# Kernel optimization log

Measured on AMD Instinct MI355X. Metric: run time of the kernel, lower is better.

## Reference

```python
import jax, jax.numpy as jnp
import numpy as np


def setup_inputs() -> dict:
    key = jax.random.key(0)
    k1, k2 = jax.random.split(key)
    B, Lp, Lw, D = 4, 256, 200, 768
    bert_emb = jax.random.normal(k1, (B, Lp, D), dtype=jnp.float32)
    # pieces2word[b, w, p] == 1 iff wordpiece p belongs to word w
    pieces2word = jax.random.randint(k2, (B, Lw, Lp), 0, 2, dtype=jnp.int32)
    return {"bert_emb": bert_emb, "pieces2word": pieces2word}


def reference(bert_emb, pieces2word):
    # Faithful to EmbeddingLayer.forward:
    #   min_value = bert_emb.min().item()  (a detached scalar in torch)
    #   _bert_embs = bert_emb.unsqueeze(1).expand(-1, Lw, -1, -1)
    #   masked_fill where pieces2word == 0 with min_value; max over piece dim
    min_value = jax.lax.stop_gradient(jnp.min(bert_emb))
    # [B, Lw, Lp, D] broadcast, masked, reduced over pieces (axis=2)
    masked = jnp.where(pieces2word[:, :, :, None] != 0,
                       bert_emb[:, None, :, :],
                       min_value)
    word_reps = jnp.max(masked, axis=2)  # [B, Lw, D]
    return word_reps
```

## Files before the change

kernel.cpp:

```cpp
#include <hip/hip_runtime.h>
#include <hip/hip_bf16.h>


#define B_  4
#define LP_ 256
#define LW_ 200
#define D_  768
#define D4_ (D_ / 4)

__device__ __forceinline__ unsigned int enc_f32(float f) {
    unsigned int b = __float_as_uint(f);
    return (b & 0x80000000u) ? ~b : (b | 0x80000000u);
}
__device__ __forceinline__ float dec_f32(unsigned int u) {
    unsigned int b = (u & 0x80000000u) ? (u & 0x7FFFFFFFu) : ~u;
    return __uint_as_float(b);
}

__global__ void init_ws(unsigned int* ws) {
    if (threadIdx.x == 0) ws[0] = 0xFFFFFFFFu;
}

__global__ void min_reduce(const float4* __restrict__ x, int n4, unsigned int* ws) {
    float m = __uint_as_float(0x7F800000u);
    for (int i = blockIdx.x * blockDim.x + threadIdx.x; i < n4;
         i += gridDim.x * blockDim.x) {
        float4 v = x[i];
        m = fminf(m, fminf(fminf(v.x, v.y), fminf(v.z, v.w)));
    }
    #pragma unroll
    for (int off = 32; off > 0; off >>= 1)
        m = fminf(m, __shfl_down(m, off, 64));
    __shared__ float sm[4];
    int lane = threadIdx.x & 63, wid = threadIdx.x >> 6;
    if (lane == 0) sm[wid] = m;
    __syncthreads();
    if (threadIdx.x == 0) {
        float bm = sm[0];
        int nw = blockDim.x >> 6;
        for (int w = 1; w < nw; ++w) bm = fminf(bm, sm[w]);
        atomicMin(ws, enc_f32(bm));
    }
}

__device__ __forceinline__ float4 max4(float4 a, float4 b) {
    return make_float4(fmaxf(a.x, b.x), fmaxf(a.y, b.y),
                       fmaxf(a.z, b.z), fmaxf(a.w, b.w));
}

__global__ __launch_bounds__(192) void word_max(
    const float* __restrict__ emb, const int* __restrict__ p2w,
    const unsigned int* __restrict__ ws, float* __restrict__ out)
{
    const int bw = blockIdx.x;
    const int b = bw / LW_;
    const int w = bw - b * LW_;

    __shared__ int   active[LP_];
    __shared__ int   s_cnt;
    __shared__ float s_minv;
    if (threadIdx.x == 0) { s_cnt = 0; s_minv = dec_f32(ws[0]); }
    __syncthreads();

    const int* mrow = p2w + (b * LW_ + w) * LP_;
    for (int p = threadIdx.x; p < LP_; p += blockDim.x) {
        if (mrow[p] != 0) {
            int slot = atomicAdd(&s_cnt, 1);
            active[slot] = p;
        }
    }
    __syncthreads();

    const float  minv = s_minv;
    const int    n    = s_cnt;
    const int    dv   = threadIdx.x;
    const float4* erow = (const float4*)(emb + b * LP_ * D_);

    float4 acc = make_float4(minv, minv, minv, minv);

    int i = 0;
    for (; i + 4 <= n; i += 4) {
        int p0 = active[i + 0];
        int p1 = active[i + 1];
        int p2 = active[i + 2];
        int p3 = active[i + 3];
        float4 v0 = erow[p0 * D4_ + dv];
        float4 v1 = erow[p1 * D4_ + dv];
        float4 v2 = erow[p2 * D4_ + dv];
        float4 v3 = erow[p3 * D4_ + dv];
        acc = max4(acc, max4(max4(v0, v1), max4(v2, v3)));
    }
    for (; i < n; ++i) {
        acc = max4(acc, erow[active[i] * D4_ + dv]);
    }

    ((float4*)out)[(b * LW_ + w) * D4_ + dv] = acc;
}

extern "C" void kernel_launch(void* const* d_in, const int* in_sizes, int n_in,
                              void* d_out, int out_size, void* d_ws, size_t ws_size,
                              hipStream_t stream) {
    const float* emb = (const float*)d_in[0];
    const int*   p2w = (const int*)d_in[1];
    float*       out = (float*)d_out;
    unsigned int* ws = (unsigned int*)d_ws;

    init_ws<<<1, 64, 0, stream>>>(ws);

    const int n4 = (B_ * LP_ * D_) / 4;
    min_reduce<<<256, 256, 0, stream>>>((const float4*)emb, n4, ws);

    word_max<<<B_ * LW_, 192, 0, stream>>>(emb, p2w, ws, out);
}
```

Baseline: 78.25 us.

## Replace atomic min with per-block partials and ballot-based mask compaction

Drops the init kernel and the global atomicMin by having 64 min blocks write partial minima, which each word_max block then reduces itself with a wavefront shuffle. The active-piece list is built with ballot/popcount prefix sums instead of shared-memory atomics, and it keeps the piece order. word_max now runs 256 threads so each thread checks one mask entry, with 64 threads idle during the max loop. This removes one launch and the atomic contention, at the cost of a redundant 64-value reduction in every block and lower per-block occupancy efficiency.

```diff
diff --git a/kernel.cpp b/kernel.cpp
--- a/kernel.cpp
+++ b/kernel.cpp
@@ -7,21 +7,12 @@
 #define LW_ 200
 #define D_  768
 #define D4_ (D_ / 4)
+#define NMIN_BLOCKS 64
 
-__device__ __forceinline__ unsigned int enc_f32(float f) {
-    unsigned int b = __float_as_uint(f);
-    return (b & 0x80000000u) ? ~b : (b | 0x80000000u);
-}
-__device__ __forceinline__ float dec_f32(unsigned int u) {
-    unsigned int b = (u & 0x80000000u) ? (u & 0x7FFFFFFFu) : ~u;
-    return __uint_as_float(b);
-}
-
-__global__ void init_ws(unsigned int* ws) {
-    if (threadIdx.x == 0) ws[0] = 0xFFFFFFFFu;
-}
-
-__global__ void min_reduce(const float4* __restrict__ x, int n4, unsigned int* ws) {
+__global__ __launch_bounds__(256) void block_min(
+    const float4* __restrict__ x, float* __restrict__ ws)
+{
+    const int n4 = (B_ * LP_ * D_) / 4;
     float m = __uint_as_float(0x7F800000u);
     for (int i = blockIdx.x * blockDim.x + threadIdx.x; i < n4;
          i += gridDim.x * blockDim.x) {
@@ -36,10 +27,8 @@
     if (lane == 0) sm[wid] = m;
     __syncthreads();
     if (threadIdx.x == 0) {
-        float bm = sm[0];
-        int nw = blockDim.x >> 6;
-        for (int w = 1; w < nw; ++w) bm = fminf(bm, sm[w]);
-        atomicMin(ws, enc_f32(bm));
+        float bm = fminf(fminf(sm[0], sm[1]), fminf(sm[2], sm[3]));
+        ws[blockIdx.x] = bm;
     }
 }
 
@@ -48,34 +37,48 @@
                        fmaxf(a.z, b.z), fmaxf(a.w, b.w));
 }
 
-__global__ __launch_bounds__(192) void word_max(
+__global__ __launch_bounds__(256) void word_max(
     const float* __restrict__ emb, const int* __restrict__ p2w,
-    const unsigned int* __restrict__ ws, float* __restrict__ out)
+    const float* __restrict__ ws, float* __restrict__ out)
 {
     const int bw = blockIdx.x;
     const int b = bw / LW_;
     const int w = bw - b * LW_;
+    const int tid = threadIdx.x;
+    const int lane = tid & 63, wid = tid >> 6;
 
     __shared__ int   active[LP_];
-    __shared__ int   s_cnt;
+    __shared__ int   wcnt[4];
     __shared__ float s_minv;
-    if (threadIdx.x == 0) { s_cnt = 0; s_minv = dec_f32(ws[0]); }
+
+    if (wid == 0) {
+        float m = ws[lane];
+        #pragma unroll
+        for (int off = 32; off > 0; off >>= 1)
+            m = fminf(m, __shfl_down(m, off, 64));
+        if (lane == 0) s_minv = m;
+    }
+
+    const int* mrow = p2w + (b * LW_ + w) * LP_;
+    const bool act = (mrow[tid] != 0);
+    const unsigned long long bal = __ballot(act);
+    if (lane == 0) wcnt[wid] = __popcll(bal);
     __syncthreads();
 
-    const int* mrow = p2w + (b * LW_ + w) * LP_;
-    for (int p = threadIdx.x; p < LP_; p += blockDim.x) {
-        if (mrow[p] != 0) {
-            int slot = atomicAdd(&s_cnt, 1);
-            active[slot] = p;
-        }
+    int off = 0;
+    #pragma unroll
+    for (int i = 0; i < 4; ++i) off += (i < wid) ? wcnt[i] : 0;
+    if (act) {
+        int pos = off + __popcll(bal & ((1ull << lane) - 1ull));
+        active[pos] = tid;
     }
+    const int n = wcnt[0] + wcnt[1] + wcnt[2] + wcnt[3];
     __syncthreads();
 
+    if (tid >= D4_) return;
+
     const float  minv = s_minv;
-    const int    n    = s_cnt;
-    const int    dv   = threadIdx.x;
     const float4* erow = (const float4*)(emb + b * LP_ * D_);
-
     float4 acc = make_float4(minv, minv, minv, minv);
 
     int i = 0;
@@ -84,17 +87,17 @@
         int p1 = active[i + 1];
         int p2 = active[i + 2];
         int p3 = active[i + 3];
-        float4 v0 = erow[p0 * D4_ + dv];
-        float4 v1 = erow[p1 * D4_ + dv];
-        float4 v2 = erow[p2 * D4_ + dv];
-        float4 v3 = erow[p3 * D4_ + dv];
+        float4 v0 = erow[p0 * D4_ + tid];
+        float4 v1 = erow[p1 * D4_ + tid];
+        float4 v2 = erow[p2 * D4_ + tid];
+        float4 v3 = erow[p3 * D4_ + tid];
         acc = max4(acc, max4(max4(v0, v1), max4(v2, v3)));
     }
     for (; i < n; ++i) {
-        acc = max4(acc, erow[active[i] * D4_ + dv]);
+        acc = max4(acc, erow[active[i] * D4_ + tid]);
     }
 
-    ((float4*)out)[(b * LW_ + w) * D4_ + dv] = acc;
+    ((float4*)out)[(b * LW_ + w) * D4_ + tid] = acc;
 }
 
 extern "C" void kernel_launch(void* const* d_in, const int* in_sizes, int n_in,
@@ -103,12 +106,8 @@
     const float* emb = (const float*)d_in[0];
     const int*   p2w = (const int*)d_in[1];
     float*       out = (float*)d_out;
-    unsigned int* ws = (unsigned int*)d_ws;
+    float*       ws  = (float*)d_ws;
 
-    init_ws<<<1, 64, 0, stream>>>(ws);
-
-    const int n4 = (B_ * LP_ * D_) / 4;
-    min_reduce<<<256, 256, 0, stream>>>((const float4*)emb, n4, ws);
-
-    word_max<<<B_ * LW_, 192, 0, stream>>>(emb, p2w, ws, out);
+    block_min<<<NMIN_BLOCKS, 256, 0, stream>>>((const float4*)emb, ws);
+    word_max<<<B_ * LW_, 256, 0, stream>>>(emb, p2w, ws, out);
 }
```

Result: no change. 77.21 us (-1.3%).
